# Kernel tuning notes

Hardware: AMD Instinct MI355X
Metric: run time of the kernel (lower is better)

## Reference

```python
import jax, jax.numpy as jnp
import numpy as np

N, A, B, C = 256, 1024, 64, 16


def setup_inputs() -> dict:
    key = jax.random.key(0)
    k1, k2, k3 = jax.random.split(key, 3)
    x = jax.random.normal(k1, (N, A), dtype=jnp.float32)
    weight = jax.random.normal(k2, (A, B * C), dtype=jnp.float32) * 0.02
    bias = jax.random.normal(k3, (B,), dtype=jnp.float32) * 0.02
    return {"x": x, "weight": weight, "bias": bias}


def reference(x, weight, bias):
    # x: [N, A]; weight: [A, B*C]; bias: [B]
    n = x.shape[0]
    mat = (x @ weight).reshape(n, B, C)              # [N, B, C]
    # pairwise L1 over the C (kernel) axis -> [N, N, B]
    l1 = jnp.abs(mat[:, None, :, :] - mat[None, :, :, :]).sum(axis=-1)
    # exp(-L1), sum over the first (broadcast) axis as in the torch code,
    # which includes the self term exp(0)=1
    out = jnp.exp(-l1).sum(axis=0) + bias            # [N, B]
    return out
```

## Files before the change

### kernel.cpp

```cpp
#include <hip/hip_runtime.h>

#define LOG2E 1.4426950408889634f

typedef __bf16 bf16x8 __attribute__((ext_vector_type(8)));
typedef float  f32x4  __attribute__((ext_vector_type(4)));

__device__ inline unsigned short f2bf(float f){
  unsigned u = __float_as_uint(f);
  unsigned r = u + 0x7FFFu + ((u >> 16) & 1u);
  return (unsigned short)(r >> 16);
}
__device__ inline unsigned pack2(float lo, float hi){
  return (unsigned)f2bf(lo) | ((unsigned)f2bf(hi) << 16);
}

__global__ __launch_bounds__(256) void k_gemm_ks(const float* __restrict__ X,
                                                 const float* __restrict__ Wm,
                                                 float* __restrict__ P){
  __shared__ unsigned short As[64 * 72];
  __shared__ unsigned short Bs[64 * 72];
  const int m0 = blockIdx.x * 64, n0 = blockIdx.y * 64;
  const int k0 = blockIdx.z * 256;
  const int t = threadIdx.x;
  const int lane = t & 63, w = t >> 6;
  const int wrow = (w & 1) * 32, wcol = (w >> 1) * 32;
  const int r16 = lane & 15, quad = lane >> 4;

  const int ar = t >> 2, aq = t & 3;
  const int bc = t & 15, bg = t >> 4;
  const float* ap = X + (size_t)(m0 + ar) * 1024 + k0 + aq * 16;
  const float* bp = Wm + (size_t)k0 * 1024 + n0 + bc * 4;

  f32x4 acc[2][2];
  #pragma unroll
  for (int p = 0; p < 2; ++p)
    #pragma unroll
    for (int q = 0; q < 2; ++q)
      #pragma unroll
      for (int e = 0; e < 4; ++e) acc[p][q][e] = 0.f;

  float4 pa[4], pb[4];
  #pragma unroll
  for (int r = 0; r < 4; ++r) pa[r] = *(const float4*)(ap + r * 4);
  #pragma unroll
  for (int r = 0; r < 4; ++r) pb[r] = *(const float4*)(bp + (size_t)(4 * bg + r) * 1024);

  #pragma unroll
  for (int kt = 0; kt < 256; kt += 64){
    __syncthreads();
    {
      unsigned short* d = &As[ar * 72 + aq * 16];
      uint4 o;
      o.x = pack2(pa[0].x, pa[0].y); o.y = pack2(pa[0].z, pa[0].w);
      o.z = pack2(pa[1].x, pa[1].y); o.w = pack2(pa[1].z, pa[1].w);
      *(uint4*)d = o;
      o.x = pack2(pa[2].x, pa[2].y); o.y = pack2(pa[2].z, pa[2].w);
      o.z = pack2(pa[3].x, pa[3].y); o.w = pack2(pa[3].z, pa[3].w);
      *(uint4*)(d + 8) = o;
    }
    {
      #pragma unroll
      for (int e = 0; e < 4; ++e){
        const int n = bc * 4 + e;
        uint2 o;
        o.x = pack2(((const float*)&pb[0])[e], ((const float*)&pb[1])[e]);
        o.y = pack2(((const float*)&pb[2])[e], ((const float*)&pb[3])[e]);
        const int cw = (bg >> 1) ^ ((n >> 3) & 7);
        *(uint2*)(&Bs[n * 72 + cw * 8 + (bg & 1) * 4]) = o;
      }
    }
    __syncthreads();
    if (kt < 192){
      #pragma unroll
      for (int r = 0; r < 4; ++r) pa[r] = *(const float4*)(ap + kt + 64 + r * 4);
      #pragma unroll
      for (int r = 0; r < 4; ++r) pb[r] = *(const float4*)(bp + (size_t)(kt + 64 + 4 * bg + r) * 1024);
    }
    #pragma unroll
    for (int kk = 0; kk < 2; ++kk){
      const int ko = kk * 32 + quad * 8;
      bf16x8 a0 = *(const bf16x8*)(&As[(wrow      + r16) * 72 + ko]);
      bf16x8 a1 = *(const bf16x8*)(&As[(wrow + 16 + r16) * 72 + ko]);
      const int c = kk * 4 + quad;
      const int nb0 = wcol + r16, nb1 = wcol + 16 + r16;
      bf16x8 b0 = *(const bf16x8*)(&Bs[nb0 * 72 + ((c ^ ((nb0 >> 3) & 7)) * 8)]);
      bf16x8 b1 = *(const bf16x8*)(&Bs[nb1 * 72 + ((c ^ ((nb1 >> 3) & 7)) * 8)]);
      acc[0][0] = __builtin_amdgcn_mfma_f32_16x16x32_bf16(a0, b0, acc[0][0], 0, 0, 0);
      acc[0][1] = __builtin_amdgcn_mfma_f32_16x16x32_bf16(a0, b1, acc[0][1], 0, 0, 0);
      acc[1][0] = __builtin_amdgcn_mfma_f32_16x16x32_bf16(a1, b0, acc[1][0], 0, 0, 0);
      acc[1][1] = __builtin_amdgcn_mfma_f32_16x16x32_bf16(a1, b1, acc[1][1], 0, 0, 0);
    }
  }
  float* Pz = P + (size_t)blockIdx.z * 256 * 1024;
  #pragma unroll
  for (int p = 0; p < 2; ++p)
    #pragma unroll
    for (int q = 0; q < 2; ++q)
      #pragma unroll
      for (int r = 0; r < 4; ++r){
        const int row = m0 + wrow + p * 16 + quad * 4 + r;
        const int col = n0 + wcol + q * 16 + r16;
        Pz[(size_t)row * 1024 + col] = acc[p][q][r];
      }
}

__global__ __launch_bounds__(1024) void k_pair(const float* __restrict__ P,
                                               const float* __restrict__ bias,
                                               float* __restrict__ out){
  __shared__ float L[256 * 16];
  __shared__ float red[16][64];
  const int b = blockIdx.x >> 2, jc = blockIdx.x & 3;
  const int t = threadIdx.x, lane = t & 63, w = t >> 6;

  {
    const int i = t >> 2, q = t & 3;
    const float* base = P + (size_t)i * 1024 + b * 16 + q * 4;
    float4 s0 = *(const float4*)(base);
    float4 s1 = *(const float4*)(base + 256 * 1024);
    float4 s2 = *(const float4*)(base + 512 * 1024);
    float4 s3 = *(const float4*)(base + 768 * 1024);
    float4 r;
    r.x = (s0.x + s1.x) + (s2.x + s3.x);
    r.y = (s0.y + s1.y) + (s2.y + s3.y);
    r.z = (s0.z + s1.z) + (s2.z + s3.z);
    r.w = (s0.w + s1.w) + (s2.w + s3.w);
    *(float4*)(&L[i * 16 + q * 4]) = r;
  }
  __syncthreads();

  const int j = jc * 64 + lane;
  float oj[16];
  #pragma unroll
  for (int q = 0; q < 4; ++q){
    float4 v = *(const float4*)(&L[j * 16 + q * 4]);
    oj[q*4+0] = v.x; oj[q*4+1] = v.y; oj[q*4+2] = v.z; oj[q*4+3] = v.w;
  }

  float acc = 0.f;
  const int i0 = w * 16;
  #pragma unroll 4
  for (int ii = i0; ii < i0 + 16; ++ii){
    const float4* fr = (const float4*)(&L[ii * 16]);
    float4 f0 = fr[0], f1 = fr[1], f2 = fr[2], f3 = fr[3];
    float p0 = fabsf(oj[0]  - f0.x) + fabsf(oj[1]  - f0.y)
             + fabsf(oj[2]  - f0.z) + fabsf(oj[3]  - f0.w);
    float p1 = fabsf(oj[4]  - f1.x) + fabsf(oj[5]  - f1.y)
             + fabsf(oj[6]  - f1.z) + fabsf(oj[7]  - f1.w);
    float p2 = fabsf(oj[8]  - f2.x) + fabsf(oj[9]  - f2.y)
             + fabsf(oj[10] - f2.z) + fabsf(oj[11] - f2.w);
    float p3 = fabsf(oj[12] - f3.x) + fabsf(oj[13] - f3.y)
             + fabsf(oj[14] - f3.z) + fabsf(oj[15] - f3.w);
    acc += exp2f(-LOG2E * ((p0 + p1) + (p2 + p3)));
  }
  red[w][lane] = acc;
  __syncthreads();
  if (w == 0){
    float tot = 0.f;
    #pragma unroll
    for (int ww = 0; ww < 16; ++ww) tot += red[ww][lane];
    out[(size_t)j * 64 + b] = tot + bias[b];
  }
}

extern "C" void kernel_launch(void* const* d_in, const int* in_sizes, int n_in,
                              void* d_out, int out_size, void* d_ws, size_t ws_size,
                              hipStream_t stream){
  const float* x    = (const float*)d_in[0];
  const float* W    = (const float*)d_in[1];
  const float* bias = (const float*)d_in[2];
  float* out = (float*)d_out;
  float* P   = (float*)d_ws;

  k_gemm_ks<<<dim3(4, 16, 4), 256, 0, stream>>>(x, W, P);
  k_pair<<<256, 1024, 0, stream>>>(P, bias, out);
}
```

Measured before the change: 76.56 us.

## Fuse GEMM and pairwise L1-exp reduction into one per-feature kernel

Replaces the split-K GEMM kernel and the separate pairwise kernel with a single kernel. Each block owns one B feature group and half of the j range. It stages that group's 16 weight columns in LDS as bf16, runs MFMA over the full K for all 256 rows, and keeps the result in LDS for the pairwise L1/exp reduction. This removes the workspace round-trip, the split-K partial sums and one launch. In exchange every block recomputes the full 256x16 GEMM slice (two blocks per feature group duplicate it) and reads all of X from global memory, with only 128 blocks in the grid.

```diff
diff --git a/kernel.cpp b/kernel.cpp
--- a/kernel.cpp
+++ b/kernel.cpp
@@ -1,146 +1,84 @@
 #include <hip/hip_runtime.h>
+#include <hip/hip_bf16.h>
 
 #define LOG2E 1.4426950408889634f
 
 typedef __bf16 bf16x8 __attribute__((ext_vector_type(8)));
 typedef float  f32x4  __attribute__((ext_vector_type(4)));
 
-__device__ inline unsigned short f2bf(float f){
-  unsigned u = __float_as_uint(f);
-  unsigned r = u + 0x7FFFu + ((u >> 16) & 1u);
-  return (unsigned short)(r >> 16);
-}
-__device__ inline unsigned pack2(float lo, float hi){
-  return (unsigned)f2bf(lo) | ((unsigned)f2bf(hi) << 16);
+__device__ inline unsigned cvt2(float lo, float hi){
+  __hip_bfloat162 h = __float22bfloat162_rn(make_float2(lo, hi));
+  return *reinterpret_cast<unsigned*>(&h);
 }
 
-__global__ __launch_bounds__(256) void k_gemm_ks(const float* __restrict__ X,
-                                                 const float* __restrict__ Wm,
-                                                 float* __restrict__ P){
-  __shared__ unsigned short As[64 * 72];
-  __shared__ unsigned short Bs[64 * 72];
-  const int m0 = blockIdx.x * 64, n0 = blockIdx.y * 64;
-  const int k0 = blockIdx.z * 256;
-  const int t = threadIdx.x;
-  const int lane = t & 63, w = t >> 6;
-  const int wrow = (w & 1) * 32, wcol = (w >> 1) * 32;
+__global__ __launch_bounds__(1024) void k_fused(const float* __restrict__ X,
+                                                const float* __restrict__ Wm,
+                                                const float* __restrict__ bias,
+                                                float* __restrict__ out){
+  __shared__ unsigned short Bs[16 * 1024];
+  __shared__ float L[256 * 20];
+  __shared__ float red[8][128];
+
+  const int b  = blockIdx.x >> 1;
+  const int jh = blockIdx.x & 1;
+  const int t = threadIdx.x, lane = t & 63, w = t >> 6;
   const int r16 = lane & 15, quad = lane >> 4;
 
-  const int ar = t >> 2, aq = t & 3;
-  const int bc = t & 15, bg = t >> 4;
-  const float* ap = X + (size_t)(m0 + ar) * 1024 + k0 + aq * 16;
-  const float* bp = Wm + (size_t)k0 * 1024 + n0 + bc * 4;
-
-  f32x4 acc[2][2];
-  #pragma unroll
-  for (int p = 0; p < 2; ++p)
+  {
+    const int kp = t & 511, ch = t >> 9;
+    const int k0 = kp * 2;
+    const int kb = k0 >> 3, ks8 = (k0 & 7);
+    const float* wp = Wm + (size_t)k0 * 1024 + b * 16 + ch * 8;
+    float4 w00 = *(const float4*)(wp);
+    float4 w01 = *(const float4*)(wp + 4);
+    float4 w10 = *(const float4*)(wp + 1024);
+    float4 w11 = *(const float4*)(wp + 1028);
+    const float* a0 = (const float*)&w00;
+    const float* a1 = (const float*)&w10;
+    const float* c0 = (const float*)&w01;
+    const float* c1 = (const float*)&w11;
     #pragma unroll
-    for (int q = 0; q < 2; ++q)
-      #pragma unroll
-      for (int e = 0; e < 4; ++e) acc[p][q][e] = 0.f;
-
-  float4 pa[4], pb[4];
-  #pragma unroll
-  for (int r = 0; r < 4; ++r) pa[r] = *(const float4*)(ap + r * 4);
-  #pragma unroll
-  for (int r = 0; r < 4; ++r) pb[r] = *(const float4*)(bp + (size_t)(4 * bg + r) * 1024);
-
-  #pragma unroll
-  for (int kt = 0; kt < 256; kt += 64){
-    __syncthreads();
-    {
-      unsigned short* d = &As[ar * 72 + aq * 16];
-      uint4 o;
-      o.x = pack2(pa[0].x, pa[0].y); o.y = pack2(pa[0].z, pa[0].w);
-      o.z = pack2(pa[1].x, pa[1].y); o.w = pack2(pa[1].z, pa[1].w);
-      *(uint4*)d = o;
-      o.x = pack2(pa[2].x, pa[2].y); o.y = pack2(pa[2].z, pa[2].w);
-      o.z = pack2(pa[3].x, pa[3].y); o.w = pack2(pa[3].z, pa[3].w);
-      *(uint4*)(d + 8) = o;
+    for (int e = 0; e < 4; ++e){
+      const int ca = ch * 8 + e;
+      *(unsigned*)&Bs[kb * 128 + ((ca ^ (kb & 7)) * 8) + ks8] = cvt2(a0[e], a1[e]);
+      const int cb = ch * 8 + 4 + e;
+      *(unsigned*)&Bs[kb * 128 + ((cb ^ (kb & 7)) * 8) + ks8] = cvt2(c0[e], c1[e]);
     }
-    {
-      #pragma unroll
-      for (int e = 0; e < 4; ++e){
-        const int n = bc * 4 + e;
-        uint2 o;
-        o.x = pack2(((const float*)&pb[0])[e], ((const float*)&pb[1])[e]);
-        o.y = pack2(((const float*)&pb[2])[e], ((const float*)&pb[3])[e]);
-        const int cw = (bg >> 1) ^ ((n >> 3) & 7);
-        *(uint2*)(&Bs[n * 72 + cw * 8 + (bg & 1) * 4]) = o;
-      }
-    }
-    __syncthreads();
-    if (kt < 192){
-      #pragma unroll
-      for (int r = 0; r < 4; ++r) pa[r] = *(const float4*)(ap + kt + 64 + r * 4);
-      #pragma unroll
-      for (int r = 0; r < 4; ++r) pb[r] = *(const float4*)(bp + (size_t)(kt + 64 + 4 * bg + r) * 1024);
-    }
-    #pragma unroll
-    for (int kk = 0; kk < 2; ++kk){
-      const int ko = kk * 32 + quad * 8;
-      bf16x8 a0 = *(const bf16x8*)(&As[(wrow      + r16) * 72 + ko]);
-      bf16x8 a1 = *(const bf16x8*)(&As[(wrow + 16 + r16) * 72 + ko]);
-      const int c = kk * 4 + quad;
-      const int nb0 = wcol + r16, nb1 = wcol + 16 + r16;
-      bf16x8 b0 = *(const bf16x8*)(&Bs[nb0 * 72 + ((c ^ ((nb0 >> 3) & 7)) * 8)]);
-      bf16x8 b1 = *(const bf16x8*)(&Bs[nb1 * 72 + ((c ^ ((nb1 >> 3) & 7)) * 8)]);
-      acc[0][0] = __builtin_amdgcn_mfma_f32_16x16x32_bf16(a0, b0, acc[0][0], 0, 0, 0);
-      acc[0][1] = __builtin_amdgcn_mfma_f32_16x16x32_bf16(a0, b1, acc[0][1], 0, 0, 0);
-      acc[1][0] = __builtin_amdgcn_mfma_f32_16x16x32_bf16(a1, b0, acc[1][0], 0, 0, 0);
-      acc[1][1] = __builtin_amdgcn_mfma_f32_16x16x32_bf16(a1, b1, acc[1][1], 0, 0, 0);
-    }
-  }
-  float* Pz = P + (size_t)blockIdx.z * 256 * 1024;
-  #pragma unroll
-  for (int p = 0; p < 2; ++p)
-    #pragma unroll
-    for (int q = 0; q < 2; ++q)
-      #pragma unroll
-      for (int r = 0; r < 4; ++r){
-        const int row = m0 + wrow + p * 16 + quad * 4 + r;
-        const int col = n0 + wcol + q * 16 + r16;
-        Pz[(size_t)row * 1024 + col] = acc[p][q][r];
-      }
-}
-
-__global__ __launch_bounds__(1024) void k_pair(const float* __restrict__ P,
-                                               const float* __restrict__ bias,
-                                               float* __restrict__ out){
-  __shared__ float L[256 * 16];
-  __shared__ float red[16][64];
-  const int b = blockIdx.x >> 2, jc = blockIdx.x & 3;
-  const int t = threadIdx.x, lane = t & 63, w = t >> 6;
-
-  {
-    const int i = t >> 2, q = t & 3;
-    const float* base = P + (size_t)i * 1024 + b * 16 + q * 4;
-    float4 s0 = *(const float4*)(base);
-    float4 s1 = *(const float4*)(base + 256 * 1024);
-    float4 s2 = *(const float4*)(base + 512 * 1024);
-    float4 s3 = *(const float4*)(base + 768 * 1024);
-    float4 r;
-    r.x = (s0.x + s1.x) + (s2.x + s3.x);
-    r.y = (s0.y + s1.y) + (s2.y + s3.y);
-    r.z = (s0.z + s1.z) + (s2.z + s3.z);
-    r.w = (s0.w + s1.w) + (s2.w + s3.w);
-    *(float4*)(&L[i * 16 + q * 4]) = r;
   }
   __syncthreads();
 
-  const int j = jc * 64 + lane;
+  f32x4 acc;
+  acc[0] = acc[1] = acc[2] = acc[3] = 0.f;
+  const float* xp = X + (size_t)(w * 16 + r16) * 1024 + quad * 8;
+  #pragma unroll 4
+  for (int ks = 0; ks < 32; ++ks){
+    float4 x0 = *(const float4*)(xp + ks * 32);
+    float4 x1 = *(const float4*)(xp + ks * 32 + 4);
+    union { unsigned u[4]; bf16x8 v; } A;
+    A.u[0] = cvt2(x0.x, x0.y); A.u[1] = cvt2(x0.z, x0.w);
+    A.u[2] = cvt2(x1.x, x1.y); A.u[3] = cvt2(x1.z, x1.w);
+    const int kb = ks * 4 + quad;
+    bf16x8 Bf = *(const bf16x8*)&Bs[kb * 128 + ((r16 ^ (kb & 7)) * 8)];
+    acc = __builtin_amdgcn_mfma_f32_16x16x32_bf16(A.v, Bf, acc, 0, 0, 0);
+  }
+  #pragma unroll
+  for (int r = 0; r < 4; ++r)
+    L[(w * 16 + quad * 4 + r) * 20 + r16] = acc[r];
+  __syncthreads();
+
+  const int jg = w & 1, ig = w >> 1;
+  const int j = jh * 128 + jg * 64 + lane;
   float oj[16];
   #pragma unroll
   for (int q = 0; q < 4; ++q){
-    float4 v = *(const float4*)(&L[j * 16 + q * 4]);
+    float4 v = *(const float4*)(&L[j * 20 + q * 4]);
     oj[q*4+0] = v.x; oj[q*4+1] = v.y; oj[q*4+2] = v.z; oj[q*4+3] = v.w;
   }
-
-  float acc = 0.f;
-  const int i0 = w * 16;
+  float accs = 0.f;
+  const int i0 = ig * 32;
   #pragma unroll 4
-  for (int ii = i0; ii < i0 + 16; ++ii){
-    const float4* fr = (const float4*)(&L[ii * 16]);
+  for (int ii = i0; ii < i0 + 32; ++ii){
+    const float4* fr = (const float4*)(&L[ii * 20]);
     float4 f0 = fr[0], f1 = fr[1], f2 = fr[2], f3 = fr[3];
     float p0 = fabsf(oj[0]  - f0.x) + fabsf(oj[1]  - f0.y)
              + fabsf(oj[2]  - f0.z) + fabsf(oj[3]  - f0.w);
@@ -150,15 +88,15 @@
              + fabsf(oj[10] - f2.z) + fabsf(oj[11] - f2.w);
     float p3 = fabsf(oj[12] - f3.x) + fabsf(oj[13] - f3.y)
              + fabsf(oj[14] - f3.z) + fabsf(oj[15] - f3.w);
-    acc += exp2f(-LOG2E * ((p0 + p1) + (p2 + p3)));
+    accs += exp2f(-LOG2E * ((p0 + p1) + (p2 + p3)));
   }
-  red[w][lane] = acc;
+  red[ig][jg * 64 + lane] = accs;
   __syncthreads();
-  if (w == 0){
+  if (t < 128){
     float tot = 0.f;
     #pragma unroll
-    for (int ww = 0; ww < 16; ++ww) tot += red[ww][lane];
-    out[(size_t)j * 64 + b] = tot + bias[b];
+    for (int p = 0; p < 8; ++p) tot += red[p][t];
+    out[(size_t)(jh * 128 + t) * 64 + b] = tot + bias[b];
   }
 }
 
@@ -169,8 +107,7 @@
   const float* W    = (const float*)d_in[1];
   const float* bias = (const float*)d_in[2];
   float* out = (float*)d_out;
-  float* P   = (float*)d_ws;
+  (void)d_ws; (void)ws_size;
 
-  k_gemm_ks<<<dim3(4, 16, 4), 256, 0, stream>>>(x, W, P);
-  k_pair<<<256, 1024, 0, stream>>>(P, bias, out);
+  k_fused<<<dim3(128), dim3(1024), 0, stream>>>(x, W, bias, out);
 }
```

After: 101.2 us. 32.2% more time.
